# Kernel optimization log

Hardware: AMD Instinct MI355X
Metric: run time of the kernel (lower is better)

## Reference

```python
import jax, jax.numpy as jnp
import numpy as np

N = 100000   # nodes
E = 600000   # edges
G = 4096     # graphs in batch
D_IN = 73
D_E = 101
D = 128      # latent_dim
BN_EPS = 1e-5


def _bn(h, gamma, beta):
    # BatchNorm1d in training mode: batch statistics (biased variance)
    m = h.mean(axis=0)
    v = h.var(axis=0)
    return (h - m) * jax.lax.rsqrt(v + BN_EPS) * gamma + beta


def setup_inputs() -> dict:
    key = jax.random.key(0)
    ks = jax.random.split(key, 24)
    inp = {
        "x": jax.random.normal(ks[0], (N, D_IN), jnp.float32),
        "edge_attr": jax.random.normal(ks[1], (E, D_E), jnp.float32),
        "src": jax.random.randint(ks[2], (E,), 0, N, jnp.int32),
        "dst": jax.random.randint(ks[3], (E,), 0, N, jnp.int32),
        "batch": jnp.sort(jax.random.randint(ks[4], (N,), 0, G, jnp.int32)),
        # node embedding Linear(73 -> 128)
        "W_emb": jax.random.normal(ks[5], (D_IN, D), jnp.float32) / np.sqrt(D_IN),
        "b_emb": jnp.zeros((D,), jnp.float32),
    }
    k = 6
    for i in range(2):
        inp[f"We{i}"] = jax.random.normal(ks[k], (D_E, D), jnp.float32) / np.sqrt(D_E); k += 1
        inp[f"be{i}"] = jnp.zeros((D,), jnp.float32)
        inp[f"W1_{i}"] = jax.random.normal(ks[k], (D, 2 * D), jnp.float32) / np.sqrt(D); k += 1
        inp[f"b1_{i}"] = jnp.zeros((2 * D,), jnp.float32)
        inp[f"g1_{i}"] = jnp.ones((2 * D,), jnp.float32)
        inp[f"bb1_{i}"] = jnp.zeros((2 * D,), jnp.float32)
        inp[f"W2_{i}"] = jax.random.normal(ks[k], (2 * D, D), jnp.float32) / np.sqrt(2 * D); k += 1
        inp[f"b2_{i}"] = jnp.zeros((D,), jnp.float32)
        inp[f"go_{i}"] = jnp.ones((D,), jnp.float32)
        inp[f"bo_{i}"] = jnp.zeros((D,), jnp.float32)
    return inp


def _forward(x, edge_attr, src, dst, batch,
             W_emb, b_emb,
             We0, be0, W1_0, b1_0, g1_0, bb1_0, W2_0, b2_0, go_0, bo_0,
             We1, be1, W1_1, b1_1, g1_1, bb1_1, W2_1, b2_1, go_1, bo_1):
    layers = [
        (We0, be0, W1_0, b1_0, g1_0, bb1_0, W2_0, b2_0, go_0, bo_0),
        (We1, be1, W1_1, b1_1, g1_1, bb1_1, W2_1, b2_1, go_1, bo_1),
    ]
    h = x @ W_emb + b_emb  # [N, D]
    n_layers = len(layers)
    for i, (We, be, W1, b1, g1, bb1, W2, b2, go, bo) in enumerate(layers):
        e = edge_attr @ We + be                         # [E, D]
        msg = jax.nn.relu(h[src] + e)                   # gather + add + ReLU
        agg = jax.ops.segment_sum(msg, dst, num_segments=N)  # scatter-sum
        z = h + agg                                     # (1 + eps) * x_i + aggr, eps = 0
        z = jax.nn.relu(_bn(z @ W1 + b1, g1, bb1))      # MLP: Linear -> BN -> ReLU
        h = _bn(z @ W2 + b2, go, bo)                    # Linear -> outer BN
        if i != n_layers - 1:
            h = jax.nn.relu(h)
        # dropout p=0 -> identity
    # global mean pool over graphs
    sums = jax.ops.segment_sum(h, batch, num_segments=G)            # [G, D]
    counts = jax.ops.segment_sum(jnp.ones((h.shape[0],), h.dtype), batch, num_segments=G)
    return sums / jnp.maximum(counts, 1.0)[:, None]


def reference(x, edge_attr, src, dst, batch,
              W_emb, b_emb,
              We0, be0, W1_0, b1_0, g1_0, bb1_0, W2_0, b2_0, go_0, bo_0,
              We1, be1, W1_1, b1_1, g1_1, bb1_1, W2_1, b2_1, go_1, bo_1):
    return _forward(x, edge_attr, src, dst, batch, W_emb, b_emb,
                    We0, be0, W1_0, b1_0, g1_0, bb1_0, W2_0, b2_0, go_0, bo_0,
                    We1, be1, W1_1, b1_1, g1_1, bb1_1, W2_1, b2_1, go_1, bo_1)
```

## Files before the change

### kernel.cpp

```cpp
#include <hip/hip_runtime.h>
#include <cstddef>

#define NN  100000
#define NE  600000
#define NG  4096
#define DIN 73
#define DE  101
#define DD  128
#define DD2 256
#define NP  100096
#define EP  600064

typedef unsigned int uint;
typedef unsigned short ushort;
typedef __attribute__((ext_vector_type(8))) short bf16x8;
typedef __attribute__((ext_vector_type(4))) float f32x4;

__device__ __forceinline__ void fadd_atomic(float* p, float v) { unsafeAtomicAdd(p, v); }

__device__ __forceinline__ ushort f2bf(float f) {
    uint u = __float_as_uint(f);
    uint r = (u + 0x7fffu + ((u >> 16) & 1u)) >> 16;
    return (ushort)r;
}
__device__ __forceinline__ float bf2f(ushort u) { return __uint_as_float(((uint)u) << 16); }


__global__ void hist_kernel(const int* __restrict__ dst, int* __restrict__ deg) {
    int e = blockIdx.x * blockDim.x + threadIdx.x;
    if (e < NE) atomicAdd(&deg[dst[e]], 1);
}

__global__ __launch_bounds__(256) void scan_chunk_kernel(
    const int* __restrict__ deg, int* __restrict__ offs, int* __restrict__ csums)
{
    const int b = blockIdx.x, t = threadIdx.x;
    const int base = b * 1024 + t * 4;
    int v[4];
    #pragma unroll
    for (int i = 0; i < 4; ++i) v[i] = (base + i < NN) ? deg[base + i] : 0;
    int tsum = v[0] + v[1] + v[2] + v[3];
    const int lane = t & 63, w = t >> 6;
    int x = tsum;
    #pragma unroll
    for (int d = 1; d < 64; d <<= 1) {
        int y = __shfl_up(x, d, 64);
        if (lane >= d) x += y;
    }
    __shared__ int wsum[4];
    if (lane == 63) wsum[w] = x;
    __syncthreads();
    int woff = 0;
    for (int i = 0; i < w; ++i) woff += wsum[i];
    int run = woff + x - tsum;
    #pragma unroll
    for (int i = 0; i < 4; ++i) {
        if (base + i < NN) offs[base + i] = run;
        run += v[i];
    }
    if (t == 255) csums[b] = woff + x;
}

__global__ void scan_tops_kernel(int* __restrict__ csums, int* __restrict__ offs, int nchunks) {
    if (threadIdx.x == 0 && blockIdx.x == 0) {
        int run = 0;
        for (int i = 0; i < nchunks; ++i) { int c = csums[i]; csums[i] = run; run += c; }
        offs[NN] = run;
    }
}

__global__ void scan_add_kernel(int* __restrict__ offs, const int* __restrict__ csums) {
    int i = blockIdx.x * blockDim.x + threadIdx.x;
    if (i < NN) offs[i] += csums[i >> 10];
}

__global__ void scatter_kernel(const int* __restrict__ dst, const int* __restrict__ offs,
                               int* __restrict__ cursor, int* __restrict__ csr)
{
    int e = blockIdx.x * blockDim.x + threadIdx.x;
    if (e >= NE) return;
    int d = dst[e];
    int pos = offs[d] + atomicAdd(&cursor[d], 1);
    csr[pos] = e;
}

__global__ void gstart_kernel(const int* __restrict__ batch, int* __restrict__ gstart) {
    int n = blockIdx.x * blockDim.x + threadIdx.x;
    if (n > NN) return;
    if (n == NN) {
        for (int g = batch[NN - 1] + 1; g <= NG; ++g) gstart[g] = NN;
        return;
    }
    int b = batch[n];
    int pb = (n == 0) ? -1 : batch[n - 1];
    for (int g = pb + 1; g <= b; ++g) gstart[g] = n;
}


__global__ __launch_bounds__(256) void cvt_ea_kernel(const float* __restrict__ ea,
                                                     ushort* __restrict__ eab)
{
    const int t = threadIdx.x;
    const int r = blockIdx.x * 8 + (t >> 5);
    if (r >= NE) return;
    const int c = (t & 31) * 4;
    ushort4 o;
    o.x = (c + 0 < DE) ? f2bf(ea[(size_t)r * DE + c + 0]) : (ushort)0;
    o.y = (c + 1 < DE) ? f2bf(ea[(size_t)r * DE + c + 1]) : (ushort)0;
    o.z = (c + 2 < DE) ? f2bf(ea[(size_t)r * DE + c + 2]) : (ushort)0;
    o.w = (c + 3 < DE) ? f2bf(ea[(size_t)r * DE + c + 3]) : (ushort)0;
    *(ushort4*)&eab[(size_t)r * 128 + c] = o;
}

__global__ void cvt_wt_kernel(const float* __restrict__ in, ushort* __restrict__ out,
                              int Kin, int Nn, int Kp)
{
    const int n = blockIdx.x;
    for (int k = threadIdx.x; k < Kp; k += blockDim.x)
        out[(size_t)n * Kp + k] = (k < Kin) ? f2bf(in[(size_t)k * Nn + n]) : (ushort)0;
}

template<int K>
__device__ __forceinline__ void mma_core(const ushort* __restrict__ Wt,
                                         const ushort* __restrict__ X,
                                         int n0, int m0, f32x4 acc[4][8])
{
    const int lane = threadIdx.x & 63;
    const int l15 = lane & 15, grp = lane >> 4;
    const size_t aoff = (size_t)(n0 + l15) * K + grp * 8;
    const size_t boff = (size_t)(m0 + l15) * K + grp * 8;
    #pragma unroll
    for (int kk = 0; kk < K / 32; ++kk) {
        bf16x8 a[8], b[4];
        #pragma unroll
        for (int nf = 0; nf < 8; ++nf)
            a[nf] = *(const bf16x8*)(Wt + aoff + (size_t)nf * 16 * K + kk * 32);
        #pragma unroll
        for (int mf = 0; mf < 4; ++mf)
            b[mf] = *(const bf16x8*)(X + boff + (size_t)mf * 16 * K + kk * 32);
        #pragma unroll
        for (int mf = 0; mf < 4; ++mf)
            #pragma unroll
            for (int nf = 0; nf < 8; ++nf)
                acc[mf][nf] = __builtin_amdgcn_mfma_f32_16x16x32_bf16(a[nf], b[mf], acc[mf][nf], 0, 0, 0);
    }
}

__device__ __forceinline__ void acc_zero(f32x4 acc[4][8]) {
    #pragma unroll
    for (int i = 0; i < 4; ++i)
        #pragma unroll
        for (int j = 0; j < 8; ++j)
            acc[i][j] = (f32x4){0.f, 0.f, 0.f, 0.f};
}

__global__ __launch_bounds__(256) void edge_gemm_kernel(
    const ushort* __restrict__ eab, const ushort* __restrict__ Wt,
    const float* __restrict__ be, const int* __restrict__ src,
    const float* __restrict__ h, ushort* __restrict__ msg)
{
    f32x4 acc[4][8];
    acc_zero(acc);
    const int e0 = blockIdx.x * 256 + (threadIdx.x >> 6) * 64;
    mma_core<128>(Wt, eab, 0, e0, acc);
    const int lane = threadIdx.x & 63, l15 = lane & 15, grp = lane >> 4;
    float4 bev[8];
    #pragma unroll
    for (int nf = 0; nf < 8; ++nf) bev[nf] = *(const float4*)&be[nf * 16 + grp * 4];
    #pragma unroll
    for (int mf = 0; mf < 4; ++mf) {
        const int e = e0 + mf * 16 + l15;
        const int sn = src[min(e, NE - 1)];
        const float* hp = &h[(size_t)sn * 128];
        #pragma unroll
        for (int nf = 0; nf < 8; ++nf) {
            const int nb = nf * 16 + grp * 4;
            const float4 hv = *(const float4*)&hp[nb];
            ushort4 o;
            o.x = f2bf(fmaxf(acc[mf][nf][0] + bev[nf].x + hv.x, 0.f));
            o.y = f2bf(fmaxf(acc[mf][nf][1] + bev[nf].y + hv.y, 0.f));
            o.z = f2bf(fmaxf(acc[mf][nf][2] + bev[nf].z + hv.z, 0.f));
            o.w = f2bf(fmaxf(acc[mf][nf][3] + bev[nf].w + hv.w, 0.f));
            *(ushort4*)&msg[(size_t)e * 128 + nb] = o;
        }
    }
}

__global__ __launch_bounds__(256) void mlp1_gemm_kernel(
    const ushort* __restrict__ z, const ushort* __restrict__ Wt,
    const float* __restrict__ bias, ushort* __restrict__ y)
{
    f32x4 acc[4][8];
    acc_zero(acc);
    const int m0 = blockIdx.x * 256 + (threadIdx.x >> 6) * 64;
    const int n0 = blockIdx.y * 128;
    mma_core<128>(Wt, z, n0, m0, acc);
    const int lane = threadIdx.x & 63, l15 = lane & 15, grp = lane >> 4;
    #pragma unroll
    for (int nf = 0; nf < 8; ++nf) {
        const int nb = n0 + nf * 16 + grp * 4;
        const float4 bv = *(const float4*)&bias[nb];
        #pragma unroll
        for (int mf = 0; mf < 4; ++mf) {
            const size_t m = m0 + mf * 16 + l15;
            ushort4 o;
            o.x = f2bf(acc[mf][nf][0] + bv.x);
            o.y = f2bf(acc[mf][nf][1] + bv.y);
            o.z = f2bf(acc[mf][nf][2] + bv.z);
            o.w = f2bf(acc[mf][nf][3] + bv.w);
            *(ushort4*)&y[m * 256 + nb] = o;
        }
    }
}

__global__ __launch_bounds__(256) void mlp2_gemm_kernel(
    const ushort* __restrict__ y1, const ushort* __restrict__ Wt,
    const float* __restrict__ bias, float* __restrict__ y2)
{
    f32x4 acc[4][8];
    acc_zero(acc);
    const int m0 = blockIdx.x * 256 + (threadIdx.x >> 6) * 64;
    mma_core<256>(Wt, y1, 0, m0, acc);
    const int lane = threadIdx.x & 63, l15 = lane & 15, grp = lane >> 4;
    #pragma unroll
    for (int nf = 0; nf < 8; ++nf) {
        const int nb = nf * 16 + grp * 4;
        const float4 bv = *(const float4*)&bias[nb];
        #pragma unroll
        for (int mf = 0; mf < 4; ++mf) {
            const size_t m = m0 + mf * 16 + l15;
            float4 o;
            o.x = acc[mf][nf][0] + bv.x;
            o.y = acc[mf][nf][1] + bv.y;
            o.z = acc[mf][nf][2] + bv.z;
            o.w = acc[mf][nf][3] + bv.w;
            *(float4*)&y2[m * 128 + nb] = o;
        }
    }
}


__global__ __launch_bounds__(128) void embed_kernel(
    const float* __restrict__ x, const float* __restrict__ W,
    const float* __restrict__ b, float* __restrict__ h)
{
    __shared__ float xs[4][DIN];
    const int n0 = blockIdx.x * 4;
    const int d  = threadIdx.x;
    for (int idx = d; idx < 4 * DIN; idx += 128) {
        int r = idx / DIN, c = idx - r * DIN;
        xs[r][c] = x[(size_t)n0 * DIN + idx];
    }
    __syncthreads();
    float bb = b[d];
    float a0 = bb, a1 = bb, a2 = bb, a3 = bb;
    for (int k = 0; k < DIN; ++k) {
        float w = W[k * DD + d];
        a0 = fmaf(xs[0][k], w, a0);
        a1 = fmaf(xs[1][k], w, a1);
        a2 = fmaf(xs[2][k], w, a2);
        a3 = fmaf(xs[3][k], w, a3);
    }
    h[(size_t)(n0 + 0) * DD + d] = a0;
    h[(size_t)(n0 + 1) * DD + d] = a1;
    h[(size_t)(n0 + 2) * DD + d] = a2;
    h[(size_t)(n0 + 3) * DD + d] = a3;
}

__global__ __launch_bounds__(256) void agg_kernel(
    const int* __restrict__ offs, const int* __restrict__ csr,
    const ushort* __restrict__ msgb, const float* __restrict__ h,
    ushort* __restrict__ zb)
{
    const int n = blockIdx.x * 4 + (threadIdx.x >> 6);
    if (n >= NN) return;
    const int lane = threadIdx.x & 63;
    const int s = offs[n], t = offs[n + 1];
    float a0 = 0.f, a1 = 0.f;
    for (int i = s; i < t; ++i) {
        const int e = csr[i];
        const uint mv = *(const uint*)&msgb[(size_t)e * 128 + lane * 2];
        a0 += __uint_as_float(mv << 16);
        a1 += __uint_as_float(mv & 0xffff0000u);
    }
    const float2 hv = *(const float2*)&h[(size_t)n * 128 + lane * 2];
    ushort2 o;
    o.x = f2bf(hv.x + a0);
    o.y = f2bf(hv.y + a1);
    *(ushort2*)&zb[(size_t)n * 128 + lane * 2] = o;
}

__global__ __launch_bounds__(256) void colstats256_kernel(
    const ushort* __restrict__ y, float* __restrict__ s, float* __restrict__ q)
{
    const int t = threadIdx.x;
    const int cs = (t & 63) * 4, rg = t >> 6;
    const int r0 = blockIdx.x * 256;
    float ps0 = 0, ps1 = 0, ps2 = 0, ps3 = 0, pq0 = 0, pq1 = 0, pq2 = 0, pq3 = 0;
    for (int i = rg; i < 256; i += 4) {
        const int r = r0 + i;
        if (r >= NN) break;
        ushort4 u = *(const ushort4*)&y[(size_t)r * 256 + cs];
        float f0 = bf2f(u.x), f1 = bf2f(u.y), f2v = bf2f(u.z), f3 = bf2f(u.w);
        ps0 += f0; pq0 += f0 * f0;
        ps1 += f1; pq1 += f1 * f1;
        ps2 += f2v; pq2 += f2v * f2v;
        ps3 += f3; pq3 += f3 * f3;
    }
    __shared__ float SS[4][256], SQ[4][256];
    SS[rg][cs + 0] = ps0; SS[rg][cs + 1] = ps1; SS[rg][cs + 2] = ps2; SS[rg][cs + 3] = ps3;
    SQ[rg][cs + 0] = pq0; SQ[rg][cs + 1] = pq1; SQ[rg][cs + 2] = pq2; SQ[rg][cs + 3] = pq3;
    __syncthreads();
    if (rg == 0) {
        #pragma unroll
        for (int j = 0; j < 4; ++j) {
            const int c = cs + j;
            fadd_atomic(&s[c], SS[0][c] + SS[1][c] + SS[2][c] + SS[3][c]);
            fadd_atomic(&q[c], SQ[0][c] + SQ[1][c] + SQ[2][c] + SQ[3][c]);
        }
    }
}

__global__ __launch_bounds__(256) void colstats128_kernel(
    const float* __restrict__ y, float* __restrict__ s, float* __restrict__ q)
{
    const int t = threadIdx.x;
    const int cs = (t & 31) * 4, rg = t >> 5;
    const int r0 = blockIdx.x * 256;
    float ps0 = 0, ps1 = 0, ps2 = 0, ps3 = 0, pq0 = 0, pq1 = 0, pq2 = 0, pq3 = 0;
    for (int i = rg; i < 256; i += 8) {
        const int r = r0 + i;
        if (r >= NN) break;
        float4 v = *(const float4*)&y[(size_t)r * 128 + cs];
        ps0 += v.x; pq0 += v.x * v.x;
        ps1 += v.y; pq1 += v.y * v.y;
        ps2 += v.z; pq2 += v.z * v.z;
        ps3 += v.w; pq3 += v.w * v.w;
    }
    __shared__ float SS[8][128], SQ[8][128];
    SS[rg][cs + 0] = ps0; SS[rg][cs + 1] = ps1; SS[rg][cs + 2] = ps2; SS[rg][cs + 3] = ps3;
    SQ[rg][cs + 0] = pq0; SQ[rg][cs + 1] = pq1; SQ[rg][cs + 2] = pq2; SQ[rg][cs + 3] = pq3;
    __syncthreads();
    if (rg == 0) {
        #pragma unroll
        for (int j = 0; j < 4; ++j) {
            const int c = cs + j;
            float sv = 0, qv = 0;
            #pragma unroll
            for (int g = 0; g < 8; ++g) { sv += SS[g][c]; qv += SQ[g][c]; }
            fadd_atomic(&s[c], sv);
            fadd_atomic(&q[c], qv);
        }
    }
}

__global__ void finalize_kernel(const float* __restrict__ s, const float* __restrict__ sq,
                                const float* __restrict__ g, const float* __restrict__ bb,
                                float* __restrict__ a, float* __restrict__ c,
                                int dim, float invN)
{
    int d = blockIdx.x * blockDim.x + threadIdx.x;
    if (d >= dim) return;
    float m  = s[d] * invN;
    float v  = sq[d] * invN - m * m;
    float rs = rsqrtf(v + 1e-5f);
    float ai = g[d] * rs;
    a[d] = ai;
    c[d] = bb[d] - m * ai;
}

__global__ void bnrelu_bf_kernel(ushort* __restrict__ y, const float* __restrict__ a,
                                 const float* __restrict__ c)
{
    int i = blockIdx.x * blockDim.x + threadIdx.x;
    const int stride = gridDim.x * blockDim.x;
    for (; i < NN * 64; i += stride) {
        const int cb = (i & 63) * 4;
        ushort4 u = *(const ushort4*)&y[(size_t)i * 4];
        const float4 av = *(const float4*)&a[cb];
        const float4 cv = *(const float4*)&c[cb];
        ushort4 o;
        o.x = f2bf(fmaxf(fmaf(bf2f(u.x), av.x, cv.x), 0.f));
        o.y = f2bf(fmaxf(fmaf(bf2f(u.y), av.y, cv.y), 0.f));
        o.z = f2bf(fmaxf(fmaf(bf2f(u.z), av.z, cv.z), 0.f));
        o.w = f2bf(fmaxf(fmaf(bf2f(u.w), av.w, cv.w), 0.f));
        *(ushort4*)&y[(size_t)i * 4] = o;
    }
}

__global__ void bn_relu_kernel(float* __restrict__ y2h, const float* __restrict__ a2,
                               const float* __restrict__ c2, int n4)
{
    int i = blockIdx.x * blockDim.x + threadIdx.x;
    const int stride = gridDim.x * blockDim.x;
    float4* p = (float4*)y2h;
    for (; i < n4; i += stride) {
        float4 v = p[i];
        const int d0 = (i & 31) * 4;
        v.x = fmaxf(fmaf(v.x, a2[d0 + 0], c2[d0 + 0]), 0.f);
        v.y = fmaxf(fmaf(v.y, a2[d0 + 1], c2[d0 + 1]), 0.f);
        v.z = fmaxf(fmaf(v.z, a2[d0 + 2], c2[d0 + 2]), 0.f);
        v.w = fmaxf(fmaf(v.w, a2[d0 + 3], c2[d0 + 3]), 0.f);
        p[i] = v;
    }
}

__global__ __launch_bounds__(256) void pool_kernel(
    const float* __restrict__ y2, const float* __restrict__ a2, const float* __restrict__ c2,
    const int* __restrict__ gstart, float* __restrict__ out)
{
    const int g = blockIdx.x * 4 + (threadIdx.x >> 6);
    if (g >= NG) return;
    const int lane = threadIdx.x & 63;
    const int s = gstart[g], t = gstart[g + 1];
    float a0 = 0.f, a1 = 0.f;
    for (int n = s; n < t; ++n) {
        const float2 v = *(const float2*)&y2[(size_t)n * 128 + lane * 2];
        a0 += v.x; a1 += v.y;
    }
    const int d0 = lane * 2;
    float2 o;
    if (t > s) {
        const float inv = 1.0f / (float)(t - s);
        o.x = fmaf(a2[d0 + 0], a0 * inv, c2[d0 + 0]);
        o.y = fmaf(a2[d0 + 1], a1 * inv, c2[d0 + 1]);
    } else {
        o.x = 0.f; o.y = 0.f;
    }
    *(float2*)&out[(size_t)g * 128 + d0] = o;
}


extern "C" void kernel_launch(void* const* d_in, const int* in_sizes, int n_in,
                              void* d_out, int out_size, void* d_ws, size_t ws_size,
                              hipStream_t stream)
{
    (void)in_sizes; (void)n_in; (void)out_size; (void)ws_size;
    const float* x     = (const float*)d_in[0];
    const float* ea    = (const float*)d_in[1];
    const int*   src   = (const int*)d_in[2];
    const int*   dst   = (const int*)d_in[3];
    const int*   batch = (const int*)d_in[4];
    const float* W_emb = (const float*)d_in[5];
    const float* b_emb = (const float*)d_in[6];

    char* ws = (char*)d_ws;
    auto alloc = [&](size_t bytes) { void* p = ws; ws += (bytes + 255) & ~(size_t)255; return p; };

    float*  hbuf = (float*) alloc((size_t)NP * 128 * 4);
    ushort* zb   = (ushort*)alloc((size_t)NP * 128 * 2);
    ushort* eab  = (ushort*)alloc((size_t)EP * 128 * 2);
    ushort* big  = (ushort*)alloc((size_t)EP * 128 * 2);
    ushort* msgb = big;
    ushort* y1b  = big;
    int* deg    = (int*)alloc((size_t)NN * 4);
    int* offs   = (int*)alloc((size_t)(NN + 1) * 4);
    int* csr    = (int*)alloc((size_t)NE * 4);
    int* csums  = (int*)alloc(128 * 4);
    int* gstart = (int*)alloc((size_t)(NG + 1) * 4);
    ushort* Wet[2], *W1t[2], *W2t[2];
    for (int l = 0; l < 2; ++l) {
        Wet[l] = (ushort*)alloc(128 * 128 * 2);
        W1t[l] = (ushort*)alloc(256 * 128 * 2);
        W2t[l] = (ushort*)alloc(128 * 256 * 2);
    }
    float* st = (float*)alloc(2048 * 4);
    float* s1 = st,        *sq1 = st + 256, *a1 = st + 512,  *c1 = st + 768;
    float* s2 = st + 1024, *sq2 = st + 1152, *a2 = st + 1280, *c2 = st + 1408;
    float* out = (float*)d_out;

    const int NCHUNK = (NN + 1023) / 1024;

    hipMemsetAsync(deg, 0, (size_t)NN * 4, stream);
    hist_kernel<<<(NE + 255) / 256, 256, 0, stream>>>(dst, deg);
    scan_chunk_kernel<<<NCHUNK, 256, 0, stream>>>(deg, offs, csums);
    scan_tops_kernel<<<1, 1, 0, stream>>>(csums, offs, NCHUNK);
    scan_add_kernel<<<(NN + 255) / 256, 256, 0, stream>>>(offs, csums);
    hipMemsetAsync(deg, 0, (size_t)NN * 4, stream);
    scatter_kernel<<<(NE + 255) / 256, 256, 0, stream>>>(dst, offs, deg, csr);
    gstart_kernel<<<(NN + 256) / 256, 256, 0, stream>>>(batch, gstart);

    cvt_ea_kernel<<<(NE + 7) / 8, 256, 0, stream>>>(ea, eab);
    for (int l = 0; l < 2; ++l) {
        const float* const* L = (const float* const*)(d_in + 7 + l * 10);
        cvt_wt_kernel<<<128, 128, 0, stream>>>(L[0], Wet[l], 101, 128, 128);
        cvt_wt_kernel<<<256, 128, 0, stream>>>(L[2], W1t[l], 128, 256, 128);
        cvt_wt_kernel<<<128, 128, 0, stream>>>(L[6], W2t[l], 256, 128, 256);
    }

    embed_kernel<<<NN / 4, 128, 0, stream>>>(x, W_emb, b_emb, hbuf);

    for (int layer = 0; layer < 2; ++layer) {
        const float* const* L = (const float* const*)(d_in + 7 + layer * 10);
        const float* be  = L[1];
        const float* b1  = L[3];
        const float* g1  = L[4]; const float* bb1 = L[5];
        const float* b2  = L[7];
        const float* go  = L[8]; const float* bo  = L[9];

        edge_gemm_kernel<<<EP / 256, 256, 0, stream>>>(eab, Wet[layer], be, src, hbuf, msgb);
        agg_kernel<<<NN / 4, 256, 0, stream>>>(offs, csr, msgb, hbuf, zb);

        hipMemsetAsync(s1, 0, 512 * sizeof(float), stream);
        hipMemsetAsync(s2, 0, 256 * sizeof(float), stream);

        mlp1_gemm_kernel<<<dim3(NP / 256, 2), 256, 0, stream>>>(zb, W1t[layer], b1, y1b);
        colstats256_kernel<<<NP / 256, 256, 0, stream>>>(y1b, s1, sq1);
        finalize_kernel<<<1, 256, 0, stream>>>(s1, sq1, g1, bb1, a1, c1, 256, 1.0f / NN);
        bnrelu_bf_kernel<<<2048, 256, 0, stream>>>(y1b, a1, c1);
        mlp2_gemm_kernel<<<NP / 256, 256, 0, stream>>>(y1b, W2t[layer], b2, hbuf);
        colstats128_kernel<<<NP / 256, 256, 0, stream>>>(hbuf, s2, sq2);
        finalize_kernel<<<1, 128, 0, stream>>>(s2, sq2, go, bo, a2, c2, 128, 1.0f / NN);

        if (layer == 0) {
            bn_relu_kernel<<<2048, 256, 0, stream>>>(hbuf, a2, c2, NN * 128 / 4);
        } else {
            pool_kernel<<<NG / 4, 256, 0, stream>>>(hbuf, a2, c2, gstart, out);
        }
    }
}
```

Baseline: 1.228 ms.

## Fuse BN stats into GEMM epilogues, store h as bf16, scatter edges in CSR order

Several changes at once. Column sum and sum-of-squares are computed in the MLP GEMM epilogues with shuffle reductions and atomics, which removes the separate colstats kernels. The first BN+ReLU is folded into the mlp2 operand load, and the node state h is stored as bf16 instead of fp32. The edge GEMM now writes its output directly into destination-sorted CSR positions without the h gather, and the aggregation kernel adds h[src] and applies ReLU itself, reading edges contiguously. This cuts memory traffic and kernel launches, at the cost of bf16 rounding of h and more atomics.

```diff
diff --git a/kernel.cpp b/kernel.cpp
--- a/kernel.cpp
+++ b/kernel.cpp
@@ -74,14 +74,16 @@
     if (i < NN) offs[i] += csums[i >> 10];
 }
 
-__global__ void scatter_kernel(const int* __restrict__ dst, const int* __restrict__ offs,
-                               int* __restrict__ cursor, int* __restrict__ csr)
+__global__ void scatter_kernel(const int* __restrict__ dst, const int* __restrict__ src,
+                               const int* __restrict__ offs, int* __restrict__ cursor,
+                               int* __restrict__ eperm, int* __restrict__ srcp)
 {
     int e = blockIdx.x * blockDim.x + threadIdx.x;
     if (e >= NE) return;
     int d = dst[e];
     int pos = offs[d] + atomicAdd(&cursor[d], 1);
-    csr[pos] = e;
+    eperm[e] = pos;
+    srcp[pos] = src[e];
 }
 
 __global__ void gstart_kernel(const int* __restrict__ batch, int* __restrict__ gstart) {
@@ -102,13 +104,15 @@
 {
     const int t = threadIdx.x;
     const int r = blockIdx.x * 8 + (t >> 5);
-    if (r >= NE) return;
+    if (r >= EP) return;
     const int c = (t & 31) * 4;
-    ushort4 o;
-    o.x = (c + 0 < DE) ? f2bf(ea[(size_t)r * DE + c + 0]) : (ushort)0;
-    o.y = (c + 1 < DE) ? f2bf(ea[(size_t)r * DE + c + 1]) : (ushort)0;
-    o.z = (c + 2 < DE) ? f2bf(ea[(size_t)r * DE + c + 2]) : (ushort)0;
-    o.w = (c + 3 < DE) ? f2bf(ea[(size_t)r * DE + c + 3]) : (ushort)0;
+    ushort4 o = {0, 0, 0, 0};
+    if (r < NE) {
+        o.x = (c + 0 < DE) ? f2bf(ea[(size_t)r * DE + c + 0]) : (ushort)0;
+        o.y = (c + 1 < DE) ? f2bf(ea[(size_t)r * DE + c + 1]) : (ushort)0;
+        o.z = (c + 2 < DE) ? f2bf(ea[(size_t)r * DE + c + 2]) : (ushort)0;
+        o.w = (c + 3 < DE) ? f2bf(ea[(size_t)r * DE + c + 3]) : (ushort)0;
+    }
     *(ushort4*)&eab[(size_t)r * 128 + c] = o;
 }
 
@@ -156,39 +160,68 @@
 
 __global__ __launch_bounds__(256) void edge_gemm_kernel(
     const ushort* __restrict__ eab, const ushort* __restrict__ Wt,
-    const float* __restrict__ be, const int* __restrict__ src,
-    const float* __restrict__ h, ushort* __restrict__ msg)
-{
+    const float* __restrict__ be, const int* __restrict__ eperm,
+    ushort* __restrict__ ecsr)
+{
+    const int e0 = blockIdx.x * 256 + (threadIdx.x >> 6) * 64;
+    const int lane = threadIdx.x & 63, l15 = lane & 15, grp = lane >> 4;
+    int pos[4];
+    #pragma unroll
+    for (int mf = 0; mf < 4; ++mf) {
+        const int e = e0 + mf * 16 + l15;
+        pos[mf] = (e < NE) ? eperm[e] : -1;
+    }
     f32x4 acc[4][8];
     acc_zero(acc);
-    const int e0 = blockIdx.x * 256 + (threadIdx.x >> 6) * 64;
     mma_core<128>(Wt, eab, 0, e0, acc);
-    const int lane = threadIdx.x & 63, l15 = lane & 15, grp = lane >> 4;
     float4 bev[8];
     #pragma unroll
     for (int nf = 0; nf < 8; ++nf) bev[nf] = *(const float4*)&be[nf * 16 + grp * 4];
     #pragma unroll
     for (int mf = 0; mf < 4; ++mf) {
-        const int e = e0 + mf * 16 + l15;
-        const int sn = src[min(e, NE - 1)];
-        const float* hp = &h[(size_t)sn * 128];
+        if (pos[mf] < 0) continue;
+        ushort* rp = &ecsr[(size_t)pos[mf] * 128];
         #pragma unroll
         for (int nf = 0; nf < 8; ++nf) {
             const int nb = nf * 16 + grp * 4;
-            const float4 hv = *(const float4*)&hp[nb];
             ushort4 o;
-            o.x = f2bf(fmaxf(acc[mf][nf][0] + bev[nf].x + hv.x, 0.f));
-            o.y = f2bf(fmaxf(acc[mf][nf][1] + bev[nf].y + hv.y, 0.f));
-            o.z = f2bf(fmaxf(acc[mf][nf][2] + bev[nf].z + hv.z, 0.f));
-            o.w = f2bf(fmaxf(acc[mf][nf][3] + bev[nf].w + hv.w, 0.f));
-            *(ushort4*)&msg[(size_t)e * 128 + nb] = o;
-        }
-    }
+            o.x = f2bf(acc[mf][nf][0] + bev[nf].x);
+            o.y = f2bf(acc[mf][nf][1] + bev[nf].y);
+            o.z = f2bf(acc[mf][nf][2] + bev[nf].z);
+            o.w = f2bf(acc[mf][nf][3] + bev[nf].w);
+            *(ushort4*)&rp[nb] = o;
+        }
+    }
+}
+
+__global__ __launch_bounds__(256) void agg_kernel(
+    const int* __restrict__ offs, const int* __restrict__ srcp,
+    const ushort* __restrict__ ecsr, const ushort* __restrict__ hb,
+    ushort* __restrict__ zb)
+{
+    const int n = blockIdx.x * 4 + (threadIdx.x >> 6);
+    if (n >= NN) return;
+    const int lane = threadIdx.x & 63;
+    const int s = offs[n], t = offs[n + 1];
+    float a0 = 0.f, a1 = 0.f;
+    for (int i = s; i < t; ++i) {
+        const int sp = srcp[i];
+        const uint ev = *(const uint*)&ecsr[(size_t)i * 128 + lane * 2];
+        const uint hv = *(const uint*)&hb[(size_t)sp * 128 + lane * 2];
+        a0 += fmaxf(__uint_as_float(ev << 16) + __uint_as_float(hv << 16), 0.f);
+        a1 += fmaxf(__uint_as_float(ev & 0xffff0000u) + __uint_as_float(hv & 0xffff0000u), 0.f);
+    }
+    const uint hh = *(const uint*)&hb[(size_t)n * 128 + lane * 2];
+    ushort2 o;
+    o.x = f2bf(__uint_as_float(hh << 16) + a0);
+    o.y = f2bf(__uint_as_float(hh & 0xffff0000u) + a1);
+    *(ushort2*)&zb[(size_t)n * 128 + lane * 2] = o;
 }
 
 __global__ __launch_bounds__(256) void mlp1_gemm_kernel(
     const ushort* __restrict__ z, const ushort* __restrict__ Wt,
-    const float* __restrict__ bias, ushort* __restrict__ y)
+    const float* __restrict__ bias, ushort* __restrict__ y,
+    float* __restrict__ s1, float* __restrict__ sq1)
 {
     f32x4 acc[4][8];
     acc_zero(acc);
@@ -200,41 +233,112 @@
     for (int nf = 0; nf < 8; ++nf) {
         const int nb = n0 + nf * 16 + grp * 4;
         const float4 bv = *(const float4*)&bias[nb];
+        float sj[4] = {0, 0, 0, 0}, qj[4] = {0, 0, 0, 0};
         #pragma unroll
         for (int mf = 0; mf < 4; ++mf) {
-            const size_t m = m0 + mf * 16 + l15;
+            const int m = m0 + mf * 16 + l15;
+            const bool valid = m < NN;
+            float v0 = acc[mf][nf][0] + bv.x;
+            float v1 = acc[mf][nf][1] + bv.y;
+            float v2 = acc[mf][nf][2] + bv.z;
+            float v3 = acc[mf][nf][3] + bv.w;
             ushort4 o;
-            o.x = f2bf(acc[mf][nf][0] + bv.x);
-            o.y = f2bf(acc[mf][nf][1] + bv.y);
-            o.z = f2bf(acc[mf][nf][2] + bv.z);
-            o.w = f2bf(acc[mf][nf][3] + bv.w);
-            *(ushort4*)&y[m * 256 + nb] = o;
+            o.x = f2bf(v0); o.y = f2bf(v1); o.z = f2bf(v2); o.w = f2bf(v3);
+            *(ushort4*)&y[(size_t)m * 256 + nb] = o;
+            if (valid) {
+                sj[0] += v0; qj[0] += v0 * v0;
+                sj[1] += v1; qj[1] += v1 * v1;
+                sj[2] += v2; qj[2] += v2 * v2;
+                sj[3] += v3; qj[3] += v3 * v3;
+            }
+        }
+        #pragma unroll
+        for (int j = 0; j < 4; ++j) {
+            float sv = sj[j], qv = qj[j];
+            #pragma unroll
+            for (int off = 1; off < 16; off <<= 1) {
+                sv += __shfl_xor(sv, off, 16);
+                qv += __shfl_xor(qv, off, 16);
+            }
+            if (l15 == 0) { fadd_atomic(&s1[nb + j], sv); fadd_atomic(&sq1[nb + j], qv); }
         }
     }
 }
 
 __global__ __launch_bounds__(256) void mlp2_gemm_kernel(
-    const ushort* __restrict__ y1, const ushort* __restrict__ Wt,
-    const float* __restrict__ bias, float* __restrict__ y2)
+    const ushort* __restrict__ y1, const float* __restrict__ a1f, const float* __restrict__ c1f,
+    const ushort* __restrict__ Wt, const float* __restrict__ bias,
+    ushort* __restrict__ y2, float* __restrict__ s2, float* __restrict__ sq2)
 {
     f32x4 acc[4][8];
     acc_zero(acc);
     const int m0 = blockIdx.x * 256 + (threadIdx.x >> 6) * 64;
-    mma_core<256>(Wt, y1, 0, m0, acc);
     const int lane = threadIdx.x & 63, l15 = lane & 15, grp = lane >> 4;
+    const size_t aoff = (size_t)l15 * 256 + grp * 8;
+    const size_t boff = (size_t)(m0 + l15) * 256 + grp * 8;
+    #pragma unroll
+    for (int kk = 0; kk < 8; ++kk) {
+        const int kb = kk * 32 + grp * 8;
+        const float4 av0 = *(const float4*)&a1f[kb];
+        const float4 av1 = *(const float4*)&a1f[kb + 4];
+        const float4 cv0 = *(const float4*)&c1f[kb];
+        const float4 cv1 = *(const float4*)&c1f[kb + 4];
+        const float aa[8] = {av0.x, av0.y, av0.z, av0.w, av1.x, av1.y, av1.z, av1.w};
+        const float cc[8] = {cv0.x, cv0.y, cv0.z, cv0.w, cv1.x, cv1.y, cv1.z, cv1.w};
+        bf16x8 a[8], b[4];
+        #pragma unroll
+        for (int nf = 0; nf < 8; ++nf)
+            a[nf] = *(const bf16x8*)(Wt + aoff + (size_t)nf * 16 * 256 + kk * 32);
+        #pragma unroll
+        for (int mf = 0; mf < 4; ++mf) {
+            bf16x8 raw = *(const bf16x8*)(y1 + boff + (size_t)mf * 16 * 256 + kk * 32);
+            bf16x8 tb;
+            #pragma unroll
+            for (int j = 0; j < 8; ++j) {
+                float f = bf2f((ushort)raw[j]);
+                f = fmaxf(fmaf(f, aa[j], cc[j]), 0.f);
+                tb[j] = (short)f2bf(f);
+            }
+            b[mf] = tb;
+        }
+        #pragma unroll
+        for (int mf = 0; mf < 4; ++mf)
+            #pragma unroll
+            for (int nf = 0; nf < 8; ++nf)
+                acc[mf][nf] = __builtin_amdgcn_mfma_f32_16x16x32_bf16(a[nf], b[mf], acc[mf][nf], 0, 0, 0);
+    }
     #pragma unroll
     for (int nf = 0; nf < 8; ++nf) {
         const int nb = nf * 16 + grp * 4;
         const float4 bv = *(const float4*)&bias[nb];
+        float sj[4] = {0, 0, 0, 0}, qj[4] = {0, 0, 0, 0};
         #pragma unroll
         for (int mf = 0; mf < 4; ++mf) {
-            const size_t m = m0 + mf * 16 + l15;
-            float4 o;
-            o.x = acc[mf][nf][0] + bv.x;
-            o.y = acc[mf][nf][1] + bv.y;
-            o.z = acc[mf][nf][2] + bv.z;
-            o.w = acc[mf][nf][3] + bv.w;
-            *(float4*)&y2[m * 128 + nb] = o;
+            const int m = m0 + mf * 16 + l15;
+            const bool valid = m < NN;
+            float v0 = acc[mf][nf][0] + bv.x;
+            float v1 = acc[mf][nf][1] + bv.y;
+            float v2 = acc[mf][nf][2] + bv.z;
+            float v3 = acc[mf][nf][3] + bv.w;
+            ushort4 o;
+            o.x = f2bf(v0); o.y = f2bf(v1); o.z = f2bf(v2); o.w = f2bf(v3);
+            *(ushort4*)&y2[(size_t)m * 128 + nb] = o;
+            if (valid) {
+                sj[0] += v0; qj[0] += v0 * v0;
+                sj[1] += v1; qj[1] += v1 * v1;
+                sj[2] += v2; qj[2] += v2 * v2;
+                sj[3] += v3; qj[3] += v3 * v3;
+            }
+        }
+        #pragma unroll
+        for (int j = 0; j < 4; ++j) {
+            float sv = sj[j], qv = qj[j];
+            #pragma unroll
+            for (int off = 1; off < 16; off <<= 1) {
+                sv += __shfl_xor(sv, off, 16);
+                qv += __shfl_xor(qv, off, 16);
+            }
+            if (l15 == 0) { fadd_atomic(&s2[nb + j], sv); fadd_atomic(&sq2[nb + j], qv); }
         }
     }
 }
@@ -242,7 +346,7 @@
 
 __global__ __launch_bounds__(128) void embed_kernel(
     const float* __restrict__ x, const float* __restrict__ W,
-    const float* __restrict__ b, float* __restrict__ h)
+    const float* __restrict__ b, ushort* __restrict__ hb)
 {
     __shared__ float xs[4][DIN];
     const int n0 = blockIdx.x * 4;
@@ -261,97 +365,10 @@
         a2 = fmaf(xs[2][k], w, a2);
         a3 = fmaf(xs[3][k], w, a3);
     }
-    h[(size_t)(n0 + 0) * DD + d] = a0;
-    h[(size_t)(n0 + 1) * DD + d] = a1;
-    h[(size_t)(n0 + 2) * DD + d] = a2;
-    h[(size_t)(n0 + 3) * DD + d] = a3;
-}
-
-__global__ __launch_bounds__(256) void agg_kernel(
-    const int* __restrict__ offs, const int* __restrict__ csr,
-    const ushort* __restrict__ msgb, const float* __restrict__ h,
-    ushort* __restrict__ zb)
-{
-    const int n = blockIdx.x * 4 + (threadIdx.x >> 6);
-    if (n >= NN) return;
-    const int lane = threadIdx.x & 63;
-    const int s = offs[n], t = offs[n + 1];
-    float a0 = 0.f, a1 = 0.f;
-    for (int i = s; i < t; ++i) {
-        const int e = csr[i];
-        const uint mv = *(const uint*)&msgb[(size_t)e * 128 + lane * 2];
-        a0 += __uint_as_float(mv << 16);
-        a1 += __uint_as_float(mv & 0xffff0000u);
-    }
-    const float2 hv = *(const float2*)&h[(size_t)n * 128 + lane * 2];
-    ushort2 o;
-    o.x = f2bf(hv.x + a0);
-    o.y = f2bf(hv.y + a1);
-    *(ushort2*)&zb[(size_t)n * 128 + lane * 2] = o;
-}
-
-__global__ __launch_bounds__(256) void colstats256_kernel(
-    const ushort* __restrict__ y, float* __restrict__ s, float* __restrict__ q)
-{
-    const int t = threadIdx.x;
-    const int cs = (t & 63) * 4, rg = t >> 6;
-    const int r0 = blockIdx.x * 256;
-    float ps0 = 0, ps1 = 0, ps2 = 0, ps3 = 0, pq0 = 0, pq1 = 0, pq2 = 0, pq3 = 0;
-    for (int i = rg; i < 256; i += 4) {
-        const int r = r0 + i;
-        if (r >= NN) break;
-        ushort4 u = *(const ushort4*)&y[(size_t)r * 256 + cs];
-        float f0 = bf2f(u.x), f1 = bf2f(u.y), f2v = bf2f(u.z), f3 = bf2f(u.w);
-        ps0 += f0; pq0 += f0 * f0;
-        ps1 += f1; pq1 += f1 * f1;
-        ps2 += f2v; pq2 += f2v * f2v;
-        ps3 += f3; pq3 += f3 * f3;
-    }
-    __shared__ float SS[4][256], SQ[4][256];
-    SS[rg][cs + 0] = ps0; SS[rg][cs + 1] = ps1; SS[rg][cs + 2] = ps2; SS[rg][cs + 3] = ps3;
-    SQ[rg][cs + 0] = pq0; SQ[rg][cs + 1] = pq1; SQ[rg][cs + 2] = pq2; SQ[rg][cs + 3] = pq3;
-    __syncthreads();
-    if (rg == 0) {
-        #pragma unroll
-        for (int j = 0; j < 4; ++j) {
-            const int c = cs + j;
-            fadd_atomic(&s[c], SS[0][c] + SS[1][c] + SS[2][c] + SS[3][c]);
-            fadd_atomic(&q[c], SQ[0][c] + SQ[1][c] + SQ[2][c] + SQ[3][c]);
-        }
-    }
-}
-
-__global__ __launch_bounds__(256) void colstats128_kernel(
-    const float* __restrict__ y, float* __restrict__ s, float* __restrict__ q)
-{
-    const int t = threadIdx.x;
-    const int cs = (t & 31) * 4, rg = t >> 5;
-    const int r0 = blockIdx.x * 256;
-    float ps0 = 0, ps1 = 0, ps2 = 0, ps3 = 0, pq0 = 0, pq1 = 0, pq2 = 0, pq3 = 0;
-    for (int i = rg; i < 256; i += 8) {
-        const int r = r0 + i;
-        if (r >= NN) break;
-        float4 v = *(const float4*)&y[(size_t)r * 128 + cs];
-        ps0 += v.x; pq0 += v.x * v.x;
-        ps1 += v.y; pq1 += v.y * v.y;
-        ps2 += v.z; pq2 += v.z * v.z;
-        ps3 += v.w; pq3 += v.w * v.w;
-    }
-    __shared__ float SS[8][128], SQ[8][128];
-    SS[rg][cs + 0] = ps0; SS[rg][cs + 1] = ps1; SS[rg][cs + 2] = ps2; SS[rg][cs + 3] = ps3;
-    SQ[rg][cs + 0] = pq0; SQ[rg][cs + 1] = pq1; SQ[rg][cs + 2] = pq2; SQ[rg][cs + 3] = pq3;
-    __syncthreads();
-    if (rg == 0) {
-        #pragma unroll
-        for (int j = 0; j < 4; ++j) {
-            const int c = cs + j;
-            float sv = 0, qv = 0;
-            #pragma unroll
-            for (int g = 0; g < 8; ++g) { sv += SS[g][c]; qv += SQ[g][c]; }
-            fadd_atomic(&s[c], sv);
-            fadd_atomic(&q[c], qv);
-        }
-    }
+    hb[(size_t)(n0 + 0) * DD + d] = f2bf(a0);
+    hb[(size_t)(n0 + 1) * DD + d] = f2bf(a1);
+    hb[(size_t)(n0 + 2) * DD + d] = f2bf(a2);
+    hb[(size_t)(n0 + 3) * DD + d] = f2bf(a3);
 }
 
 __global__ void finalize_kernel(const float* __restrict__ s, const float* __restrict__ sq,
@@ -369,14 +386,14 @@
     c[d] = bb[d] - m * ai;
 }
 
-__global__ void bnrelu_bf_kernel(ushort* __restrict__ y, const float* __restrict__ a,
+__global__ void bnrelu_hb_kernel(ushort* __restrict__ hb, const float* __restrict__ a,
                                  const float* __restrict__ c)
 {
     int i = blockIdx.x * blockDim.x + threadIdx.x;
     const int stride = gridDim.x * blockDim.x;
-    for (; i < NN * 64; i += stride) {
-        const int cb = (i & 63) * 4;
-        ushort4 u = *(const ushort4*)&y[(size_t)i * 4];
+    for (; i < NN * 32; i += stride) {
+        const int cb = (i & 31) * 4;
+        ushort4 u = *(const ushort4*)&hb[(size_t)i * 4];
         const float4 av = *(const float4*)&a[cb];
         const float4 cv = *(const float4*)&c[cb];
         ushort4 o;
@@ -384,29 +401,12 @@
         o.y = f2bf(fmaxf(fmaf(bf2f(u.y), av.y, cv.y), 0.f));
         o.z = f2bf(fmaxf(fmaf(bf2f(u.z), av.z, cv.z), 0.f));
         o.w = f2bf(fmaxf(fmaf(bf2f(u.w), av.w, cv.w), 0.f));
-        *(ushort4*)&y[(size_t)i * 4] = o;
-    }
-}
-
-__global__ void bn_relu_kernel(float* __restrict__ y2h, const float* __restrict__ a2,
-                               const float* __restrict__ c2, int n4)
-{
-    int i = blockIdx.x * blockDim.x + threadIdx.x;
-    const int stride = gridDim.x * blockDim.x;
-    float4* p = (float4*)y2h;
-    for (; i < n4; i += stride) {
-        float4 v = p[i];
-        const int d0 = (i & 31) * 4;
-        v.x = fmaxf(fmaf(v.x, a2[d0 + 0], c2[d0 + 0]), 0.f);
-        v.y = fmaxf(fmaf(v.y, a2[d0 + 1], c2[d0 + 1]), 0.f);
-        v.z = fmaxf(fmaf(v.z, a2[d0 + 2], c2[d0 + 2]), 0.f);
-        v.w = fmaxf(fmaf(v.w, a2[d0 + 3], c2[d0 + 3]), 0.f);
-        p[i] = v;
+        *(ushort4*)&hb[(size_t)i * 4] = o;
     }
 }
 
 __global__ __launch_bounds__(256) void pool_kernel(
-    const float* __restrict__ y2, const float* __restrict__ a2, const float* __restrict__ c2,
+    const ushort* __restrict__ hb, const float* __restrict__ a2, const float* __restrict__ c2,
     const int* __restrict__ gstart, float* __restrict__ out)
 {
     const int g = blockIdx.x * 4 + (threadIdx.x >> 6);
@@ -415,8 +415,9 @@
     const int s = gstart[g], t = gstart[g + 1];
     float a0 = 0.f, a1 = 0.f;
     for (int n = s; n < t; ++n) {
-        const float2 v = *(const float2*)&y2[(size_t)n * 128 + lane * 2];
-        a0 += v.x; a1 += v.y;
+        const uint v = *(const uint*)&hb[(size_t)n * 128 + lane * 2];
+        a0 += __uint_as_float(v << 16);
+        a1 += __uint_as_float(v & 0xffff0000u);
     }
     const int d0 = lane * 2;
     float2 o;
@@ -447,15 +448,16 @@
     char* ws = (char*)d_ws;
     auto alloc = [&](size_t bytes) { void* p = ws; ws += (bytes + 255) & ~(size_t)255; return p; };
 
-    float*  hbuf = (float*) alloc((size_t)NP * 128 * 4);
-    ushort* zb   = (ushort*)alloc((size_t)NP * 128 * 2);
-    ushort* eab  = (ushort*)alloc((size_t)EP * 128 * 2);
-    ushort* big  = (ushort*)alloc((size_t)EP * 128 * 2);
-    ushort* msgb = big;
+    ushort* hb  = (ushort*)alloc((size_t)NP * 128 * 2);
+    ushort* zb  = (ushort*)alloc((size_t)NP * 128 * 2);
+    ushort* eab = (ushort*)alloc((size_t)EP * 128 * 2);
+    ushort* big = (ushort*)alloc((size_t)EP * 128 * 2);
+    ushort* ecsr = big;
     ushort* y1b  = big;
     int* deg    = (int*)alloc((size_t)NN * 4);
     int* offs   = (int*)alloc((size_t)(NN + 1) * 4);
-    int* csr    = (int*)alloc((size_t)NE * 4);
+    int* eperm  = (int*)alloc((size_t)NE * 4);
+    int* srcp   = (int*)alloc((size_t)NE * 4);
     int* csums  = (int*)alloc(128 * 4);
     int* gstart = (int*)alloc((size_t)(NG + 1) * 4);
     ushort* Wet[2], *W1t[2], *W2t[2];
@@ -477,10 +479,10 @@
     scan_tops_kernel<<<1, 1, 0, stream>>>(csums, offs, NCHUNK);
     scan_add_kernel<<<(NN + 255) / 256, 256, 0, stream>>>(offs, csums);
     hipMemsetAsync(deg, 0, (size_t)NN * 4, stream);
-    scatter_kernel<<<(NE + 255) / 256, 256, 0, stream>>>(dst, offs, deg, csr);
+    scatter_kernel<<<(NE + 255) / 256, 256, 0, stream>>>(dst, src, offs, deg, eperm, srcp);
     gstart_kernel<<<(NN + 256) / 256, 256, 0, stream>>>(batch, gstart);
 
-    cvt_ea_kernel<<<(NE + 7) / 8, 256, 0, stream>>>(ea, eab);
+    cvt_ea_kernel<<<EP / 8, 256, 0, stream>>>(ea, eab);
     for (int l = 0; l < 2; ++l) {
         const float* const* L = (const float* const*)(d_in + 7 + l * 10);
         cvt_wt_kernel<<<128, 128, 0, stream>>>(L[0], Wet[l], 101, 128, 128);
@@ -488,7 +490,7 @@
         cvt_wt_kernel<<<128, 128, 0, stream>>>(L[6], W2t[l], 256, 128, 256);
     }
 
-    embed_kernel<<<NN / 4, 128, 0, stream>>>(x, W_emb, b_emb, hbuf);
+    embed_kernel<<<NN / 4, 128, 0, stream>>>(x, W_emb, b_emb, hb);
 
     for (int layer = 0; layer < 2; ++layer) {
         const float* const* L = (const float* const*)(d_in + 7 + layer * 10);
@@ -498,24 +500,21 @@
         const float* b2  = L[7];
         const float* go  = L[8]; const float* bo  = L[9];
 
-        edge_gemm_kernel<<<EP / 256, 256, 0, stream>>>(eab, Wet[layer], be, src, hbuf, msgb);
-        agg_kernel<<<NN / 4, 256, 0, stream>>>(offs, csr, msgb, hbuf, zb);
+        edge_gemm_kernel<<<EP / 256, 256, 0, stream>>>(eab, Wet[layer], be, eperm, ecsr);
+        agg_kernel<<<NN / 4, 256, 0, stream>>>(offs, srcp, ecsr, hb, zb);
 
         hipMemsetAsync(s1, 0, 512 * sizeof(float), stream);
         hipMemsetAsync(s2, 0, 256 * sizeof(float), stream);
 
-        mlp1_gemm_kernel<<<dim3(NP / 256, 2), 256, 0, stream>>>(zb, W1t[layer], b1, y1b);
-        colstats256_kernel<<<NP / 256, 256, 0, stream>>>(y1b, s1, sq1);
+        mlp1_gemm_kernel<<<dim3(NP / 256, 2), 256, 0, stream>>>(zb, W1t[layer], b1, y1b, s1, sq1);
         finalize_kernel<<<1, 256, 0, stream>>>(s1, sq1, g1, bb1, a1, c1, 256, 1.0f / NN);
-        bnrelu_bf_kernel<<<2048, 256, 0, stream>>>(y1b, a1, c1);
-        mlp2_gemm_kernel<<<NP / 256, 256, 0, stream>>>(y1b, W2t[layer], b2, hbuf);
-        colstats128_kernel<<<NP / 256, 256, 0, stream>>>(hbuf, s2, sq2);
+        mlp2_gemm_kernel<<<NP / 256, 256, 0, stream>>>(y1b, a1, c1, W2t[layer], b2, hb, s2, sq2);
         finalize_kernel<<<1, 128, 0, stream>>>(s2, sq2, go, bo, a2, c2, 128, 1.0f / NN);
 
         if (layer == 0) {
-            bn_relu_kernel<<<2048, 256, 0, stream>>>(hbuf, a2, c2, NN * 128 / 4);
+            bnrelu_hb_kernel<<<2048, 256, 0, stream>>>(hb, a2, c2);
         } else {
-            pool_kernel<<<NG / 4, 256, 0, stream>>>(hbuf, a2, c2, gstart, out);
-        }
-    }
-}
+            pool_kernel<<<NG / 4, 256, 0, stream>>>(hb, a2, c2, gstart, out);
+        }
+    }
+}
```

Result: slower. 1.859 ms (+51.4%).
